# Kernel optimization log

Hardware: AMD Instinct MI355X
Metric: run time of the kernel (lower is better)

The kernel has to match this reference:

```python
import jax, jax.numpy as jnp
import numpy as np

ALPHA = 100.0  # superspike surrogate sharpness (fwd uses hard heaviside)
DT = 0.001
TAU_SYN_INV = 200.0
TAU_MEM_INV = 100.0
V_LEAK = 0.0
V_TH = 1.0
V_RESET = 0.0

@jax.custom_vjp
def heaviside(x):
    return (x > 0).astype(x.dtype)

def _heaviside_fwd(x):
    return heaviside(x), x

def _heaviside_bwd(x, g):
    # norse 'super' (SuperSpike) surrogate gradient
    return (g / (ALPHA * jnp.abs(x) + 1.0) ** 2,)

heaviside.defvjp(_heaviside_fwd, _heaviside_bwd)


def setup_inputs() -> dict:
    key = jax.random.key(0)
    k1, k2 = jax.random.split(key)
    T, B, F = 1024, 128, 512
    input_spikes = jax.random.uniform(k1, (T, B, F), dtype=jnp.float32)
    bound = 1.0 / np.sqrt(F)
    W = jax.random.uniform(k2, (F, F), minval=-bound, maxval=bound, dtype=jnp.float32)
    return {"input_spikes": input_spikes, "W": W}


def reference(input_spikes, W):
    # fc applied per timestep is equivalent to one batched contraction over time
    xs = jnp.einsum('tbf,gf->tbg', input_spikes, W)  # [T,B,F]
    B, F = input_spikes.shape[1], input_spikes.shape[2]

    def step(carry, x_t):
        v, i = carry
        v_decayed = v + DT * TAU_MEM_INV * ((V_LEAK - v) + i)
        i_decayed = i + (-DT * TAU_SYN_INV) * i
        z = heaviside(v_decayed - V_TH)
        v_new = (1.0 - z) * v_decayed + z * V_RESET
        i_new = i_decayed + x_t
        return (v_new, i_new), z

    init = (jnp.zeros((B, F), input_spikes.dtype), jnp.zeros((B, F), input_spikes.dtype))
    (v_final, i_final), zs = jax.lax.scan(step, init, xs)
    z_final = zs[-1]
    # original returns (z, LIFState(z, v, i))
    return z_final, z_final, v_final, i_final
```

## Files before the change

kernel.cpp:

```cpp
#include <hip/hip_runtime.h>


#define T_DIM 1024
#define B_DIM 128
#define F_DIM 512
#define NB (B_DIM * F_DIM)

#define TM 128
#define TN 256
#define KC 32
#define LDA_S 132
#define LDB_S 260

__global__ __launch_bounds__(256, 2)
void gemm_kernel(const float* __restrict__ A, const float* __restrict__ W,
                 float* __restrict__ C) {
    __shared__ float As[KC * LDA_S];
    __shared__ float Bs[KC * LDB_S];
    const int tid = threadIdx.x;
    const int m0 = blockIdx.x * TM;
    const int n0 = blockIdx.y * TN;
    const int tn4 = (tid & 15) * 4;
    const int tm4 = (tid >> 4) * 4;
    const int srow = tid >> 3;
    const int sk = (tid & 7) * 4;

    float acc[8][16];
    #pragma unroll
    for (int i = 0; i < 8; ++i)
        #pragma unroll
        for (int j = 0; j < 16; ++j) acc[i][j] = 0.f;

    float4 av[4];
    #pragma unroll
    for (int p = 0; p < 4; ++p)
        av[p] = *(const float4*)(A + (size_t)(m0 + srow + 32 * p) * F_DIM + sk);

    for (int k0 = 0; k0 < F_DIM; k0 += KC) {
        float4 bv[8];
        #pragma unroll
        for (int p = 0; p < 8; ++p)
            bv[p] = *(const float4*)(W + (size_t)(n0 + srow + 32 * p) * F_DIM + k0 + sk);
        __syncthreads();
        #pragma unroll
        for (int p = 0; p < 4; ++p) {
            const int r = srow + 32 * p;
            As[(sk + 0) * LDA_S + r] = av[p].x;  As[(sk + 1) * LDA_S + r] = av[p].y;
            As[(sk + 2) * LDA_S + r] = av[p].z;  As[(sk + 3) * LDA_S + r] = av[p].w;
        }
        #pragma unroll
        for (int p = 0; p < 8; ++p) {
            const int r = srow + 32 * p;
            Bs[(sk + 0) * LDB_S + r] = bv[p].x;  Bs[(sk + 1) * LDB_S + r] = bv[p].y;
            Bs[(sk + 2) * LDB_S + r] = bv[p].z;  Bs[(sk + 3) * LDB_S + r] = bv[p].w;
        }
        __syncthreads();

        if (k0 + KC < F_DIM) {
            #pragma unroll
            for (int p = 0; p < 4; ++p)
                av[p] = *(const float4*)(A + (size_t)(m0 + srow + 32 * p) * F_DIM
                                           + (k0 + KC) + sk);
        }

        #pragma unroll 4
        for (int k = 0; k < KC; ++k) {
            const float4 a0 = *(const float4*)(As + k * LDA_S + tm4);
            const float4 a1 = *(const float4*)(As + k * LDA_S + tm4 + 64);
            const float4 b0 = *(const float4*)(Bs + k * LDB_S + tn4);
            const float4 b1 = *(const float4*)(Bs + k * LDB_S + tn4 + 64);
            const float4 b2 = *(const float4*)(Bs + k * LDB_S + tn4 + 128);
            const float4 b3 = *(const float4*)(Bs + k * LDB_S + tn4 + 192);
            const float a[8] = {a0.x, a0.y, a0.z, a0.w, a1.x, a1.y, a1.z, a1.w};
            const float b[16] = {b0.x, b0.y, b0.z, b0.w, b1.x, b1.y, b1.z, b1.w,
                                 b2.x, b2.y, b2.z, b2.w, b3.x, b3.y, b3.z, b3.w};
            #pragma unroll
            for (int i = 0; i < 8; ++i)
                #pragma unroll
                for (int j = 0; j < 16; ++j)
                    acc[i][j] += a[i] * b[j];
        }
    }

    #pragma unroll
    for (int i = 0; i < 8; ++i) {
        const int m = m0 + ((i < 4) ? (tm4 + i) : (tm4 + 60 + i));
        #pragma unroll
        for (int q = 0; q < 4; ++q) {
            const float4 c = make_float4(acc[i][4 * q + 0], acc[i][4 * q + 1],
                                         acc[i][4 * q + 2], acc[i][4 * q + 3]);
            *(float4*)(C + (size_t)m * F_DIM + n0 + tn4 + 64 * q) = c;
        }
    }
}

#define DEPTH 32

__global__ __launch_bounds__(256)
void scan_kernel(const float* __restrict__ xs, float* __restrict__ vi,
                 float* __restrict__ out, int Tc, int first, int last) {
    const int j = blockIdx.x * 256 + threadIdx.x;
    float v, cur;
    if (first) { v = 0.f; cur = 0.f; }
    else       { v = vi[j]; cur = vi[NB + j]; }
    float z = 0.f;
    const float* pj = xs + j;

    if (Tc >= DEPTH && (Tc % DEPTH) == 0) {
        float buf[DEPTH];
        #pragma unroll
        for (int d = 0; d < DEPTH; ++d) buf[d] = pj[(size_t)d * NB];
        for (int tt = 0; tt < Tc; tt += DEPTH) {
            #pragma unroll
            for (int d = 0; d < DEPTH; ++d) {
                const float x = buf[d];
                int tn = tt + DEPTH + d;
                tn = (tn < Tc) ? tn : 0;
                buf[d] = pj[(size_t)tn * NB];
                const float vd = __fadd_rn(v, __fmul_rn(0.1f, __fsub_rn(cur, v)));
                const float id = __fadd_rn(cur, __fmul_rn(-0.2f, cur));
                const bool sp = vd > 1.0f;
                z = sp ? 1.f : 0.f;
                v = sp ? 0.f : vd;
                cur = __fadd_rn(id, x);
            }
        }
    } else {
        for (int t = 0; t < Tc; ++t) {
            const float x = pj[(size_t)t * NB];
            const float vd = __fadd_rn(v, __fmul_rn(0.1f, __fsub_rn(cur, v)));
            const float id = __fadd_rn(cur, __fmul_rn(-0.2f, cur));
            const bool sp = vd > 1.0f;
            z = sp ? 1.f : 0.f;
            v = sp ? 0.f : vd;
            cur = __fadd_rn(id, x);
        }
    }

    if (last) {
        out[j]           = z;
        out[NB + j]      = z;
        out[2 * NB + j]  = v;
        out[3 * NB + j]  = cur;
    } else {
        vi[j]      = v;
        vi[NB + j] = cur;
    }
}

extern "C" void kernel_launch(void* const* d_in, const int* in_sizes, int n_in,
                              void* d_out, int out_size, void* d_ws, size_t ws_size,
                              hipStream_t stream) {
    const float* S = (const float*)d_in[0];
    const float* W = (const float*)d_in[1];
    float* out = (float*)d_out;
    float* vi = (float*)d_ws;
    float* xs = vi + 2 * NB;
    const size_t avail_f = (ws_size / 4 > (size_t)(2 * NB)) ? ws_size / 4 - 2 * NB : 0;
    int Tc = T_DIM;
    while (Tc > 1 && (size_t)Tc * NB > avail_f) Tc >>= 1;
    if (Tc > 256) Tc = 256;
    const int nc = T_DIM / Tc;
    for (int c = 0; c < nc; ++c) {
        const int M = Tc * B_DIM;
        dim3 grid(M / TM, F_DIM / TN);
        gemm_kernel<<<grid, 256, 0, stream>>>(S + (size_t)c * Tc * NB, W, xs);
        scan_kernel<<<NB / 256, 256, 0, stream>>>(xs, vi, out, Tc,
                                                  (c == 0) ? 1 : 0,
                                                  (c == nc - 1) ? 1 : 0);
    }
}
```

Before: 1.121 ms.

## Double-buffer GEMM shared-memory tiles and drop the chunk-size cap

Shared-memory A/B tiles in the GEMM are now double-buffered with a K chunk of 16 instead of 32. Global loads for the next chunk are issued before the current chunk's FMAs, and the store into the other buffer needs only one barrier per iteration, aiming to hide load latency and halve synchronisation. The host also removes the 256-timestep cap on the chunk size, so fewer GEMM+scan launch pairs run when the workspace allows. A larger chunk needs a bigger xs workspace, and the halved K chunk means more loop iterations and barriers overall.

```diff
diff --git a/kernel.cpp b/kernel.cpp
--- a/kernel.cpp
+++ b/kernel.cpp
@@ -8,22 +8,24 @@
 
 #define TM 128
 #define TN 256
-#define KC 32
+#define KC 16
 #define LDA_S 132
 #define LDB_S 260
+#define A_SZ (KC * LDA_S)
+#define B_SZ (KC * LDB_S)
 
 __global__ __launch_bounds__(256, 2)
 void gemm_kernel(const float* __restrict__ A, const float* __restrict__ W,
                  float* __restrict__ C) {
-    __shared__ float As[KC * LDA_S];
-    __shared__ float Bs[KC * LDB_S];
+    __shared__ float As[2 * A_SZ];
+    __shared__ float Bs[2 * B_SZ];
     const int tid = threadIdx.x;
     const int m0 = blockIdx.x * TM;
     const int n0 = blockIdx.y * TN;
     const int tn4 = (tid & 15) * 4;
     const int tm4 = (tid >> 4) * 4;
-    const int srow = tid >> 3;
-    const int sk = (tid & 7) * 4;
+    const int srow = tid >> 2;
+    const int sk = (tid & 3) * 4;
 
     float acc[8][16];
     #pragma unroll
@@ -31,46 +33,54 @@
         #pragma unroll
         for (int j = 0; j < 16; ++j) acc[i][j] = 0.f;
 
-    float4 av[4];
-    #pragma unroll
-    for (int p = 0; p < 4; ++p)
-        av[p] = *(const float4*)(A + (size_t)(m0 + srow + 32 * p) * F_DIM + sk);
-
-    for (int k0 = 0; k0 < F_DIM; k0 += KC) {
-        float4 bv[8];
-        #pragma unroll
-        for (int p = 0; p < 8; ++p)
-            bv[p] = *(const float4*)(W + (size_t)(n0 + srow + 32 * p) * F_DIM + k0 + sk);
-        __syncthreads();
-        #pragma unroll
-        for (int p = 0; p < 4; ++p) {
-            const int r = srow + 32 * p;
+    {
+        float4 av[2], bv[4];
+        #pragma unroll
+        for (int p = 0; p < 2; ++p)
+            av[p] = *(const float4*)(A + (size_t)(m0 + srow + 64 * p) * F_DIM + sk);
+        #pragma unroll
+        for (int p = 0; p < 4; ++p)
+            bv[p] = *(const float4*)(W + (size_t)(n0 + srow + 64 * p) * F_DIM + sk);
+        #pragma unroll
+        for (int p = 0; p < 2; ++p) {
+            const int r = srow + 64 * p;
             As[(sk + 0) * LDA_S + r] = av[p].x;  As[(sk + 1) * LDA_S + r] = av[p].y;
             As[(sk + 2) * LDA_S + r] = av[p].z;  As[(sk + 3) * LDA_S + r] = av[p].w;
         }
         #pragma unroll
-        for (int p = 0; p < 8; ++p) {
-            const int r = srow + 32 * p;
+        for (int p = 0; p < 4; ++p) {
+            const int r = srow + 64 * p;
             Bs[(sk + 0) * LDB_S + r] = bv[p].x;  Bs[(sk + 1) * LDB_S + r] = bv[p].y;
             Bs[(sk + 2) * LDB_S + r] = bv[p].z;  Bs[(sk + 3) * LDB_S + r] = bv[p].w;
         }
         __syncthreads();
-
-        if (k0 + KC < F_DIM) {
+    }
+
+    int cur = 0;
+    for (int k0 = 0; k0 < F_DIM; k0 += KC) {
+        const bool more = (k0 + KC < F_DIM);
+        float4 av[2], bv[4];
+        if (more) {
+            #pragma unroll
+            for (int p = 0; p < 2; ++p)
+                av[p] = *(const float4*)(A + (size_t)(m0 + srow + 64 * p) * F_DIM
+                                           + (k0 + KC) + sk);
             #pragma unroll
             for (int p = 0; p < 4; ++p)
-                av[p] = *(const float4*)(A + (size_t)(m0 + srow + 32 * p) * F_DIM
+                bv[p] = *(const float4*)(W + (size_t)(n0 + srow + 64 * p) * F_DIM
                                            + (k0 + KC) + sk);
         }
 
+        const float* asb = As + cur * A_SZ;
+        const float* bsb = Bs + cur * B_SZ;
         #pragma unroll 4
         for (int k = 0; k < KC; ++k) {
-            const float4 a0 = *(const float4*)(As + k * LDA_S + tm4);
-            const float4 a1 = *(const float4*)(As + k * LDA_S + tm4 + 64);
-            const float4 b0 = *(const float4*)(Bs + k * LDB_S + tn4);
-            const float4 b1 = *(const float4*)(Bs + k * LDB_S + tn4 + 64);
-            const float4 b2 = *(const float4*)(Bs + k * LDB_S + tn4 + 128);
-            const float4 b3 = *(const float4*)(Bs + k * LDB_S + tn4 + 192);
+            const float4 a0 = *(const float4*)(asb + k * LDA_S + tm4);
+            const float4 a1 = *(const float4*)(asb + k * LDA_S + tm4 + 64);
+            const float4 b0 = *(const float4*)(bsb + k * LDB_S + tn4);
+            const float4 b1 = *(const float4*)(bsb + k * LDB_S + tn4 + 64);
+            const float4 b2 = *(const float4*)(bsb + k * LDB_S + tn4 + 128);
+            const float4 b3 = *(const float4*)(bsb + k * LDB_S + tn4 + 192);
             const float a[8] = {a0.x, a0.y, a0.z, a0.w, a1.x, a1.y, a1.z, a1.w};
             const float b[16] = {b0.x, b0.y, b0.z, b0.w, b1.x, b1.y, b1.z, b1.w,
                                  b2.x, b2.y, b2.z, b2.w, b3.x, b3.y, b3.z, b3.w};
@@ -79,6 +89,25 @@
                 #pragma unroll
                 for (int j = 0; j < 16; ++j)
                     acc[i][j] += a[i] * b[j];
+        }
+
+        if (more) {
+            float* asn = As + (cur ^ 1) * A_SZ;
+            float* bsn = Bs + (cur ^ 1) * B_SZ;
+            #pragma unroll
+            for (int p = 0; p < 2; ++p) {
+                const int r = srow + 64 * p;
+                asn[(sk + 0) * LDA_S + r] = av[p].x;  asn[(sk + 1) * LDA_S + r] = av[p].y;
+                asn[(sk + 2) * LDA_S + r] = av[p].z;  asn[(sk + 3) * LDA_S + r] = av[p].w;
+            }
+            #pragma unroll
+            for (int p = 0; p < 4; ++p) {
+                const int r = srow + 64 * p;
+                bsn[(sk + 0) * LDB_S + r] = bv[p].x;  bsn[(sk + 1) * LDB_S + r] = bv[p].y;
+                bsn[(sk + 2) * LDB_S + r] = bv[p].z;  bsn[(sk + 3) * LDB_S + r] = bv[p].w;
+            }
+            __syncthreads();
+            cur ^= 1;
         }
     }
 
@@ -159,7 +188,6 @@
     const size_t avail_f = (ws_size / 4 > (size_t)(2 * NB)) ? ws_size / 4 - 2 * NB : 0;
     int Tc = T_DIM;
     while (Tc > 1 && (size_t)Tc * NB > avail_f) Tc >>= 1;
-    if (Tc > 256) Tc = 256;
     const int nc = T_DIM / Tc;
     for (int c = 0; c < nc; ++c) {
         const int M = Tc * B_DIM;
```

After: 1.031 ms. -8.0%, faster.
